# Kernel tuning notes

Hardware: AMD Instinct MI355X
Metric: run time of the kernel (lower is better)

## Reference

```python
import jax, jax.numpy as jnp
import numpy as np

B, H, S, DK = 2, 16, 2048, 128


def setup_inputs() -> dict:
    key = jax.random.key(0)
    kq, kk, kv = jax.random.split(key, 3)
    return {
        "queries": jax.random.normal(kq, (B, H, S, DK), dtype=jnp.float32),
        "keys": jax.random.normal(kk, (B, H, S, DK), dtype=jnp.float32),
        "values": jax.random.normal(kv, (B, H, S, DK), dtype=jnp.float32),
        "d_k": DK,
    }


def reference(queries, keys, values, d_k):
    # scores: [B, H, Sq, Sk] = Q @ K^T / sqrt(d_k)
    scale = 1.0 / np.sqrt(float(d_k)).astype(np.float32)
    scores = jnp.einsum("bhqd,bhkd->bhqk", queries, keys) * scale
    weights = jax.nn.softmax(scores, axis=-1)
    return jnp.einsum("bhqk,bhkd->bhqd", weights, values)
```

## Files before the change

### kernel.cpp

```cpp
#include <hip/hip_runtime.h>
#include <hip/hip_bf16.h>

#define SREF 2048
#define DHEAD 128
#define KVBLK 64
#define NTHREADS 256
#define NTILES (SREF / KVBLK)
#define PSTR 72
#define QSCALE 0.12751743f
#define THRLOG 8.0f

typedef short bf16x8 __attribute__((ext_vector_type(8)));
typedef float f32x4 __attribute__((ext_vector_type(4)));
typedef float f32x16 __attribute__((ext_vector_type(16)));

typedef const __attribute__((address_space(1))) void* gas_t;
typedef __attribute__((address_space(3))) void* las_t;

__device__ __forceinline__ ushort f2bf(float x) {
    unsigned u = __builtin_bit_cast(unsigned, x);
    u += 0x7fffu + ((u >> 16) & 1u);
    return (ushort)(u >> 16);
}

__device__ __forceinline__ float fexp2(float x) {
#if __has_builtin(__builtin_amdgcn_exp2f)
    return __builtin_amdgcn_exp2f(x);
#else
    return exp2f(x);
#endif
}

__device__ __forceinline__ unsigned cvtpk(float lo, float hi) {
    unsigned r;
    asm("v_cvt_pk_bf16_f32 %0, %1, %2" : "=v"(r) : "v"(lo), "v"(hi));
    return r;
}

__global__ __launch_bounds__(NTHREADS) void preconv_kernel(
    const float* __restrict__ K, const float* __restrict__ V,
    ushort* __restrict__ Kb, ushort* __restrict__ VTb)
{
    __shared__ ushort T[DHEAD * PSTR];
    const int t  = threadIdx.x;
    const int bh = blockIdx.y;
    const int s0 = blockIdx.x * KVBLK;
    const size_t base = (size_t)bh * SREF * DHEAD;

    const float* kb = K + base + (size_t)s0 * DHEAD;
    ushort* kout = Kb + base + (size_t)s0 * DHEAD;
    #pragma unroll
    for (int i = 0; i < 8; ++i) {
        int idx = t + i * NTHREADS;
        float4 f = *(const float4*)(kb + idx * 4);
        ushort4 h; h.x = f2bf(f.x); h.y = f2bf(f.y); h.z = f2bf(f.z); h.w = f2bf(f.w);
        *(ushort4*)(kout + idx * 4) = h;
    }

    const float* vb = V + base + (size_t)s0 * DHEAD;
    #pragma unroll
    for (int i = 0; i < 8; ++i) {
        const int key = (t & 31) + 32 * (i & 1);
        const int d4  = (t >> 5) + 8 * (i >> 1);
        float4 f = *(const float4*)(vb + key * DHEAD + d4 * 4);
        T[(d4 * 4 + 0) * PSTR + key] = f2bf(f.x);
        T[(d4 * 4 + 1) * PSTR + key] = f2bf(f.y);
        T[(d4 * 4 + 2) * PSTR + key] = f2bf(f.z);
        T[(d4 * 4 + 3) * PSTR + key] = f2bf(f.w);
    }
    __syncthreads();

    ushort* vt = VTb + (size_t)bh * DHEAD * SREF + s0;
    #pragma unroll
    for (int i = 0; i < 4; ++i) {
        int idx = t + i * NTHREADS;
        int d = idx >> 3;
        int c = (idx & 7) * 8;
        bf16x8 v = *(const bf16x8*)&T[d * PSTR + c];
        *(bf16x8*)(vt + (size_t)d * SREF + c) = v;
    }
}

__global__ __launch_bounds__(NTHREADS, 2) void attn_fwd_kernel(
    const float* __restrict__ Q, const ushort* __restrict__ Kb,
    const ushort* __restrict__ VTb, float* __restrict__ O)
{
    __shared__ __align__(16) char smem[67584];

    const int t    = threadIdx.x;
    const int lane = t & 63;
    const int wv   = t >> 6;
    const int hi   = lane >> 5;
    const int q5   = lane & 31;
    const int swz  = (lane & 7) << 4;

    const int bh = blockIdx.y;
    const int q0 = blockIdx.x * 128;
    const size_t base = (size_t)bh * SREF * DHEAD;

    bf16x8 qf[8];
    {
        const float* qrow = Q + base + (size_t)(q0 + wv * 32 + q5) * DHEAD;
        #pragma unroll
        for (int dk = 0; dk < 8; ++dk) {
            const int d0 = dk * 16 + hi * 8;
            float4 a = *(const float4*)(qrow + d0);
            float4 b = *(const float4*)(qrow + d0 + 4);
            bf16x8 f;
            f[0] = (short)f2bf(a.x * QSCALE); f[1] = (short)f2bf(a.y * QSCALE);
            f[2] = (short)f2bf(a.z * QSCALE); f[3] = (short)f2bf(a.w * QSCALE);
            f[4] = (short)f2bf(b.x * QSCALE); f[5] = (short)f2bf(b.y * QSCALE);
            f[6] = (short)f2bf(b.z * QSCALE); f[7] = (short)f2bf(b.w * QSCALE);
            qf[dk] = f;
        }
    }

    const char* ksrcb = (const char*)(Kb + base);
    const char* vsrcb = (const char*)(VTb + (size_t)bh * DHEAD * SREF);

    const int kbaseL = q5 * 256 + ((hi * 16) ^ swz);
    const int vbaseL = q5 * 128 + ((hi * 16) ^ swz);

#define STAGE(b, kv0) do {                                                      \
    const char* kt_ = ksrcb + (size_t)(kv0) * (DHEAD * 2);                      \
    const char* vt_ = vsrcb + (size_t)(kv0) * 2;                                \
    _Pragma("unroll")                                                           \
    for (int i_ = 0; i_ < 4; ++i_) {                                            \
        int L_ = t * 16 + i_ * 4096;                                            \
        int r_ = L_ >> 8;                                                       \
        __builtin_amdgcn_global_load_lds(                                       \
            (gas_t)(const void*)(kt_ + (L_ ^ ((r_ & 7) << 4))),                 \
            (las_t)(void*)(smem + (b) * 16384 + L_), 16, 0, 0);                 \
    }                                                                           \
    _Pragma("unroll")                                                           \
    for (int i_ = 0; i_ < 4; ++i_) {                                            \
        int L_ = t * 16 + i_ * 4096;                                            \
        int d_ = L_ >> 7;                                                       \
        int c_ = L_ & 127;                                                      \
        __builtin_amdgcn_global_load_lds(                                       \
            (gas_t)(const void*)(vt_ + (size_t)d_ * (SREF * 2) + (c_ ^ ((d_ & 7) << 4))), \
            (las_t)(void*)(smem + 32768 + (b) * 16384 + L_), 16, 0, 0);         \
    }                                                                           \
} while (0)

    float mrun = -1e30f, lsum = 0.0f;
    f32x16 acc[4];
    #pragma unroll
    for (int db = 0; db < 4; ++db)
        #pragma unroll
        for (int i = 0; i < 16; ++i) acc[db][i] = 0.0f;

    STAGE(0, 0);
    int buf = 0;

    for (int tt = 0; tt < NTILES; ++tt) {
        if (tt + 1 < NTILES) {
            STAGE(buf ^ 1, (tt + 1) * KVBLK);
            asm volatile("s_waitcnt vmcnt(8)" ::: "memory");
        } else {
            asm volatile("s_waitcnt vmcnt(0)" ::: "memory");
        }
        __builtin_amdgcn_s_barrier();
        __builtin_amdgcn_sched_barrier(0);

        const int kO = buf * 16384;
        const int vO = 32768 + buf * 16384;

        f32x16 s0, s1;
        #pragma unroll
        for (int i = 0; i < 16; ++i) { s0[i] = 0.0f; s1[i] = 0.0f; }
        __builtin_amdgcn_s_setprio(1);
        #pragma unroll
        for (int dk = 0; dk < 8; ++dk) {
            bf16x8 kf0 = *(const bf16x8*)(smem + kO + (kbaseL ^ (dk << 5)));
            s0 = __builtin_amdgcn_mfma_f32_32x32x16_bf16(kf0, qf[dk], s0, 0, 0, 0);
            bf16x8 kf1 = *(const bf16x8*)(smem + kO + 8192 + (kbaseL ^ (dk << 5)));
            s1 = __builtin_amdgcn_mfma_f32_32x32x16_bf16(kf1, qf[dk], s1, 0, 0, 0);
        }
        __builtin_amdgcn_s_setprio(0);

        float pmax = s0[0];
        #pragma unroll
        for (int i = 1; i < 16; ++i) pmax = fmaxf(pmax, s0[i]);
        #pragma unroll
        for (int i = 0; i < 16; ++i) pmax = fmaxf(pmax, s1[i]);
        pmax = fmaxf(pmax, __shfl_xor(pmax, 32));

        if (!__all(pmax <= mrun + THRLOG)) {
            const float mnew  = fmaxf(mrun, pmax);
            const float alpha = fexp2(mrun - mnew);
            mrun = mnew;
            lsum *= alpha;
            #pragma unroll
            for (int db = 0; db < 4; ++db)
                #pragma unroll
                for (int i = 0; i < 16; ++i) acc[db][i] *= alpha;
        }

        float rs = 0.0f;
        #pragma unroll
        for (int i = 0; i < 16; ++i) { s0[i] = fexp2(s0[i] - mrun); rs += s0[i]; }
        #pragma unroll
        for (int i = 0; i < 16; ++i) { s1[i] = fexp2(s1[i] - mrun); rs += s1[i]; }
        rs += __shfl_xor(rs, 32);
        lsum += rs;

        bf16x8 pa[4];
        #pragma unroll
        for (int kb = 0; kb < 2; ++kb) {
            #pragma unroll
            for (int c = 0; c < 2; ++c) {
                float p0 = (kb ? s1[8*c+0] : s0[8*c+0]);
                float p1 = (kb ? s1[8*c+1] : s0[8*c+1]);
                float p2 = (kb ? s1[8*c+2] : s0[8*c+2]);
                float p3 = (kb ? s1[8*c+3] : s0[8*c+3]);
                float p4 = (kb ? s1[8*c+4] : s0[8*c+4]);
                float p5 = (kb ? s1[8*c+5] : s0[8*c+5]);
                float p6 = (kb ? s1[8*c+6] : s0[8*c+6]);
                float p7 = (kb ? s1[8*c+7] : s0[8*c+7]);
                unsigned x0 = cvtpk(p0, p1);
                unsigned x1 = cvtpk(p2, p3);
                unsigned y0 = cvtpk(p4, p5);
                unsigned y1 = cvtpk(p6, p7);
                asm volatile("v_permlane32_swap_b32 %0, %1" : "+v"(x0), "+v"(y0));
                asm volatile("v_permlane32_swap_b32 %0, %1" : "+v"(x1), "+v"(y1));
                union { unsigned u[4]; bf16x8 v; } U;
                U.u[0] = x0; U.u[1] = x1; U.u[2] = y0; U.u[3] = y1;
                pa[kb * 2 + c] = U.v;
            }
        }

        __builtin_amdgcn_s_setprio(1);
        #pragma unroll
        for (int db = 0; db < 4; ++db) {
            #pragma unroll
            for (int ks = 0; ks < 4; ++ks) {
                bf16x8 vf = *(const bf16x8*)(smem + vO + db * 4096 + (vbaseL ^ (ks << 5)));
                acc[db] = __builtin_amdgcn_mfma_f32_32x32x16_bf16(vf, pa[ks], acc[db], 0, 0, 0);
            }
        }
        __builtin_amdgcn_s_setprio(0);

        __builtin_amdgcn_sched_barrier(0);
        __builtin_amdgcn_s_barrier();
        buf ^= 1;
    }

    __syncthreads();

    const float inv = 1.0f / lsum;
    const int eb = wv * 16896;
    #pragma unroll
    for (int db = 0; db < 4; ++db) {
        #pragma unroll
        for (int c = 0; c < 4; ++c) {
            f32x4 v;
            v[0] = acc[db][4*c+0] * inv;
            v[1] = acc[db][4*c+1] * inv;
            v[2] = acc[db][4*c+2] * inv;
            v[3] = acc[db][4*c+3] * inv;
            *(f32x4*)(smem + eb + q5 * 528 + db * 128 + c * 32 + hi * 16) = v;
        }
    }
    #pragma unroll
    for (int i = 0; i < 16; ++i) {
        const int flat  = lane + i * 64;
        const int row   = flat >> 5;
        const int chunk = flat & 31;
        f32x4 v = *(const f32x4*)(smem + eb + row * 528 + chunk * 16);
        *(f32x4*)(O + base + (size_t)(q0 + wv * 32 + row) * DHEAD + chunk * 4) = v;
    }
#undef STAGE
}

__global__ __launch_bounds__(NTHREADS) void attn_fwd_fallback(
    const float* __restrict__ Q, const float* __restrict__ K,
    const float* __restrict__ V, float* __restrict__ O)
{
    __shared__ ushort Ksh[KVBLK * 136];
    __shared__ ushort Vsh[DHEAD * 72];
    __shared__ ushort Psh[4][16 * PSTR];

    const int t    = threadIdx.x;
    const int lane = t & 63;
    const int wv   = t >> 6;
    const int lq   = lane & 15;
    const int kh   = lane >> 4;

    const int bh = blockIdx.y;
    const int q0 = blockIdx.x * 64;
    const size_t base = (size_t)bh * SREF * DHEAD;

    const float scale = 0.08838834764831845f;
    bf16x8 qf[4];
    {
        const float* qrow = Q + base + (size_t)(q0 + wv * 16 + lq) * DHEAD;
        #pragma unroll
        for (int kk = 0; kk < 4; ++kk) {
            const int d0 = kk * 32 + kh * 8;
            float4 a = *(const float4*)(qrow + d0);
            float4 b = *(const float4*)(qrow + d0 + 4);
            bf16x8 f;
            f[0] = (short)f2bf(a.x * scale); f[1] = (short)f2bf(a.y * scale);
            f[2] = (short)f2bf(a.z * scale); f[3] = (short)f2bf(a.w * scale);
            f[4] = (short)f2bf(b.x * scale); f[5] = (short)f2bf(b.y * scale);
            f[6] = (short)f2bf(b.z * scale); f[7] = (short)f2bf(b.w * scale);
            qf[kk] = f;
        }
    }

    float mrun[4], lrun[4];
    f32x4 acc_o[8];
    #pragma unroll
    for (int r = 0; r < 4; ++r) { mrun[r] = -1e30f; lrun[r] = 0.0f; }
    #pragma unroll
    for (int db = 0; db < 8; ++db) acc_o[db] = (f32x4){0.f, 0.f, 0.f, 0.f};

    for (int kv0 = 0; kv0 < SREF; kv0 += KVBLK) {
        __syncthreads();
        const float* kbase = K + base + (size_t)kv0 * DHEAD;
        #pragma unroll
        for (int i = 0; i < 8; ++i) {
            const int idx = t + i * NTHREADS;
            const int row = idx >> 5;
            const int c4  = idx & 31;
            float4 f = *(const float4*)(kbase + row * DHEAD + c4 * 4);
            ushort4 h;
            h.x = f2bf(f.x); h.y = f2bf(f.y); h.z = f2bf(f.z); h.w = f2bf(f.w);
            *(ushort4*)&Ksh[row * 136 + c4 * 4] = h;
        }
        const float* vbase = V + base + (size_t)kv0 * DHEAD;
        #pragma unroll
        for (int i = 0; i < 8; ++i) {
            const int key = (t & 31) + 32 * (i & 1);
            const int d4  = (t >> 5) + 8 * (i >> 1);
            float4 f = *(const float4*)(vbase + key * DHEAD + d4 * 4);
            Vsh[(d4 * 4 + 0) * 72 + key] = f2bf(f.x);
            Vsh[(d4 * 4 + 1) * 72 + key] = f2bf(f.y);
            Vsh[(d4 * 4 + 2) * 72 + key] = f2bf(f.z);
            Vsh[(d4 * 4 + 3) * 72 + key] = f2bf(f.w);
        }
        __syncthreads();

        f32x4 accs[4];
        #pragma unroll
        for (int nb = 0; nb < 4; ++nb) accs[nb] = (f32x4){0.f, 0.f, 0.f, 0.f};
        #pragma unroll
        for (int kk = 0; kk < 4; ++kk) {
            #pragma unroll
            for (int nb = 0; nb < 4; ++nb) {
                bf16x8 kf = *(const bf16x8*)&Ksh[(nb * 16 + lq) * 136 + kk * 32 + kh * 8];
                accs[nb] = __builtin_amdgcn_mfma_f32_16x16x32_bf16(qf[kk], kf, accs[nb], 0, 0, 0);
            }
        }

        float ps[4][4];
        #pragma unroll
        for (int r = 0; r < 4; ++r) {
            float v = fmaxf(fmaxf(accs[0][r], accs[1][r]), fmaxf(accs[2][r], accs[3][r]));
            #pragma unroll
            for (int mk = 1; mk < 16; mk <<= 1) v = fmaxf(v, __shfl_xor(v, mk));
            const float mnew  = fmaxf(mrun[r], v);
            const float alpha = __expf(mrun[r] - mnew);
            mrun[r] = mnew;
            float rs = 0.0f;
            #pragma unroll
            for (int nb = 0; nb < 4; ++nb) {
                const float p = __expf(accs[nb][r] - mnew);
                ps[nb][r] = p;
                rs += p;
            }
            #pragma unroll
            for (int mk = 1; mk < 16; mk <<= 1) rs += __shfl_xor(rs, mk);
            lrun[r] = lrun[r] * alpha + rs;
            #pragma unroll
            for (int db = 0; db < 8; ++db) acc_o[db][r] *= alpha;
        }

        #pragma unroll
        for (int nb = 0; nb < 4; ++nb)
            #pragma unroll
            for (int r = 0; r < 4; ++r)
                Psh[wv][(kh * 4 + r) * PSTR + nb * 16 + lq] = f2bf(ps[nb][r]);

        #pragma unroll
        for (int ks = 0; ks < 2; ++ks) {
            bf16x8 pa = *(const bf16x8*)&Psh[wv][lq * PSTR + ks * 32 + kh * 8];
            #pragma unroll
            for (int db = 0; db < 8; ++db) {
                bf16x8 vf = *(const bf16x8*)&Vsh[(db * 16 + lq) * 72 + ks * 32 + kh * 8];
                acc_o[db] = __builtin_amdgcn_mfma_f32_16x16x32_bf16(pa, vf, acc_o[db], 0, 0, 0);
            }
        }
    }

    #pragma unroll
    for (int r = 0; r < 4; ++r) {
        const float inv = 1.0f / lrun[r];
        float* orow = O + base + (size_t)(q0 + wv * 16 + kh * 4 + r) * DHEAD;
        #pragma unroll
        for (int db = 0; db < 8; ++db)
            orow[db * 16 + lq] = acc_o[db][r] * inv;
    }
}

extern "C" void kernel_launch(void* const* d_in, const int* in_sizes, int n_in,
                              void* d_out, int out_size, void* d_ws, size_t ws_size,
                              hipStream_t stream) {
    const float* Q = (const float*)d_in[0];
    const float* K = (const float*)d_in[1];
    const float* V = (const float*)d_in[2];
    float* O = (float*)d_out;
    const int BH = in_sizes[0] / (SREF * DHEAD);
    const size_t nel = (size_t)BH * SREF * DHEAD;

    if (ws_size >= 2 * nel * sizeof(ushort)) {
        ushort* Kb  = (ushort*)d_ws;
        ushort* VTb = Kb + nel;
        preconv_kernel<<<dim3(SREF / KVBLK, BH), NTHREADS, 0, stream>>>(K, V, Kb, VTb);
        attn_fwd_kernel<<<dim3(SREF / 128, BH), NTHREADS, 0, stream>>>(Q, Kb, VTb, O);
    } else {
        attn_fwd_fallback<<<dim3(SREF / 64, BH), NTHREADS, 0, stream>>>(Q, K, V, O);
    }
}
```

Before: 100.7 us.

## Software-pipeline attention loop: overlap next QK^T with current softmax and PV

Restructures the main KV loop into a two-tile ping-pong pipeline. The QK^T MFMAs for tile t+1 are issued between the softmax and the PV MFMAs of tile t, and K and V loads are staged separately so K runs one tile ahead. The goal is to hide the softmax VALU and exp latency behind matrix work. It also splits the row-sum reduction into independent accumulators and defers the cross-half lane shuffle of lsum to the epilogue. In exchange it needs more live registers (two score sets) and a full vmcnt(0) wait at each phase, which could cut occupancy or expose load latency.

```diff
diff --git a/kernel.cpp b/kernel.cpp
--- a/kernel.cpp
+++ b/kernel.cpp
@@ -78,6 +78,67 @@
         int c = (idx & 7) * 8;
         bf16x8 v = *(const bf16x8*)&T[d * PSTR + c];
         *(bf16x8*)(vt + (size_t)d * SREF + c) = v;
+    }
+}
+
+__device__ __forceinline__ void softmax_step(
+    f32x16& s0, f32x16& s1, float& mrun, float& lsumh,
+    f32x16* acc, bf16x8* pa)
+{
+    float m0[8];
+    #pragma unroll
+    for (int i = 0; i < 8; ++i)
+        m0[i] = fmaxf(fmaxf(s0[i], s0[i + 8]), fmaxf(s1[i], s1[i + 8]));
+    float pmax = fmaxf(fmaxf(fmaxf(m0[0], m0[1]), fmaxf(m0[2], m0[3])),
+                       fmaxf(fmaxf(m0[4], m0[5]), fmaxf(m0[6], m0[7])));
+    pmax = fmaxf(pmax, __shfl_xor(pmax, 32));
+
+    if (!__all(pmax <= mrun + THRLOG)) {
+        const float mnew  = fmaxf(mrun, pmax);
+        const float alpha = fexp2(mrun - mnew);
+        mrun = mnew;
+        lsumh *= alpha;
+        #pragma unroll
+        for (int db = 0; db < 4; ++db)
+            #pragma unroll
+            for (int i = 0; i < 16; ++i) acc[db][i] *= alpha;
+    }
+
+    float r0 = 0.f, r1 = 0.f, r2 = 0.f, r3 = 0.f;
+    #pragma unroll
+    for (int i = 0; i < 16; i += 4) {
+        s0[i]   = fexp2(s0[i]   - mrun); r0 += s0[i];
+        s0[i+1] = fexp2(s0[i+1] - mrun); r1 += s0[i+1];
+        s0[i+2] = fexp2(s0[i+2] - mrun); r2 += s0[i+2];
+        s0[i+3] = fexp2(s0[i+3] - mrun); r3 += s0[i+3];
+    }
+    #pragma unroll
+    for (int i = 0; i < 16; i += 4) {
+        s1[i]   = fexp2(s1[i]   - mrun); r0 += s1[i];
+        s1[i+1] = fexp2(s1[i+1] - mrun); r1 += s1[i+1];
+        s1[i+2] = fexp2(s1[i+2] - mrun); r2 += s1[i+2];
+        s1[i+3] = fexp2(s1[i+3] - mrun); r3 += s1[i+3];
+    }
+    lsumh += (r0 + r1) + (r2 + r3);
+
+    #pragma unroll
+    for (int kb = 0; kb < 2; ++kb) {
+        #pragma unroll
+        for (int c = 0; c < 2; ++c) {
+            unsigned x0, x1, y0, y1;
+            if (kb == 0) {
+                x0 = cvtpk(s0[8*c+0], s0[8*c+1]); x1 = cvtpk(s0[8*c+2], s0[8*c+3]);
+                y0 = cvtpk(s0[8*c+4], s0[8*c+5]); y1 = cvtpk(s0[8*c+6], s0[8*c+7]);
+            } else {
+                x0 = cvtpk(s1[8*c+0], s1[8*c+1]); x1 = cvtpk(s1[8*c+2], s1[8*c+3]);
+                y0 = cvtpk(s1[8*c+4], s1[8*c+5]); y1 = cvtpk(s1[8*c+6], s1[8*c+7]);
+            }
+            asm volatile("v_permlane32_swap_b32 %0, %1" : "+v"(x0), "+v"(y0));
+            asm volatile("v_permlane32_swap_b32 %0, %1" : "+v"(x1), "+v"(y1));
+            union { unsigned u[4]; bf16x8 v; } U;
+            U.u[0] = x0; U.u[1] = x1; U.u[2] = y0; U.u[3] = y1;
+            pa[kb * 2 + c] = U.v;
+        }
     }
 }
 
@@ -121,17 +182,23 @@
     const int kbaseL = q5 * 256 + ((hi * 16) ^ swz);
     const int vbaseL = q5 * 128 + ((hi * 16) ^ swz);
 
-#define STAGE(b, kv0) do {                                                      \
+#define KOFF(b) ((b) * 16384)
+#define VOFF(b) (32768 + (b) * 16384)
+
+#define STAGE_K(b, kv0) do {                                                    \
     const char* kt_ = ksrcb + (size_t)(kv0) * (DHEAD * 2);                      \
-    const char* vt_ = vsrcb + (size_t)(kv0) * 2;                                \
     _Pragma("unroll")                                                           \
     for (int i_ = 0; i_ < 4; ++i_) {                                            \
         int L_ = t * 16 + i_ * 4096;                                            \
         int r_ = L_ >> 8;                                                       \
         __builtin_amdgcn_global_load_lds(                                       \
             (gas_t)(const void*)(kt_ + (L_ ^ ((r_ & 7) << 4))),                 \
-            (las_t)(void*)(smem + (b) * 16384 + L_), 16, 0, 0);                 \
+            (las_t)(void*)(smem + KOFF(b) + L_), 16, 0, 0);                     \
     }                                                                           \
+} while (0)
+
+#define STAGE_V(b, kv0) do {                                                    \
+    const char* vt_ = vsrcb + (size_t)(kv0) * 2;                                \
     _Pragma("unroll")                                                           \
     for (int i_ = 0; i_ < 4; ++i_) {                                            \
         int L_ = t * 16 + i_ * 4096;                                            \
@@ -139,116 +206,87 @@
         int c_ = L_ & 127;                                                      \
         __builtin_amdgcn_global_load_lds(                                       \
             (gas_t)(const void*)(vt_ + (size_t)d_ * (SREF * 2) + (c_ ^ ((d_ & 7) << 4))), \
-            (las_t)(void*)(smem + 32768 + (b) * 16384 + L_), 16, 0, 0);         \
+            (las_t)(void*)(smem + VOFF(b) + L_), 16, 0, 0);                     \
     }                                                                           \
 } while (0)
 
-    float mrun = -1e30f, lsum = 0.0f;
+#define QK_REGION(sd0, sd1, kO_) do {                                           \
+    _Pragma("unroll")                                                           \
+    for (int i_ = 0; i_ < 16; ++i_) { sd0[i_] = 0.f; sd1[i_] = 0.f; }           \
+    _Pragma("unroll")                                                           \
+    for (int dk_ = 0; dk_ < 8; ++dk_) {                                         \
+        bf16x8 kf0 = *(const bf16x8*)(smem + (kO_) + (kbaseL ^ (dk_ << 5)));    \
+        sd0 = __builtin_amdgcn_mfma_f32_32x32x16_bf16(kf0, qf[dk_], sd0, 0, 0, 0); \
+        bf16x8 kf1 = *(const bf16x8*)(smem + (kO_) + 8192 + (kbaseL ^ (dk_ << 5))); \
+        sd1 = __builtin_amdgcn_mfma_f32_32x32x16_bf16(kf1, qf[dk_], sd1, 0, 0, 0); \
+    }                                                                           \
+} while (0)
+
+#define PV_REGION(pa_, vO_) do {                                                \
+    __builtin_amdgcn_s_setprio(1);                                              \
+    _Pragma("unroll")                                                           \
+    for (int db_ = 0; db_ < 4; ++db_) {                                         \
+        _Pragma("unroll")                                                       \
+        for (int ks_ = 0; ks_ < 4; ++ks_) {                                     \
+            bf16x8 vf = *(const bf16x8*)(smem + (vO_) + db_ * 4096 + (vbaseL ^ (ks_ << 5))); \
+            acc[db_] = __builtin_amdgcn_mfma_f32_32x32x16_bf16(vf, pa_[ks_], acc[db_], 0, 0, 0); \
+        }                                                                       \
+    }                                                                           \
+    __builtin_amdgcn_s_setprio(0);                                              \
+} while (0)
+
+#define PHASE_SYNC() do {                                                       \
+    asm volatile("s_waitcnt vmcnt(0)" ::: "memory");                            \
+    __builtin_amdgcn_s_barrier();                                               \
+    __builtin_amdgcn_sched_barrier(0);                                          \
+} while (0)
+
+    float mrun = -1e30f, lsumh = 0.0f;
     f32x16 acc[4];
     #pragma unroll
     for (int db = 0; db < 4; ++db)
         #pragma unroll
         for (int i = 0; i < 16; ++i) acc[db][i] = 0.0f;
 
-    STAGE(0, 0);
-    int buf = 0;
-
-    for (int tt = 0; tt < NTILES; ++tt) {
-        if (tt + 1 < NTILES) {
-            STAGE(buf ^ 1, (tt + 1) * KVBLK);
-            asm volatile("s_waitcnt vmcnt(8)" ::: "memory");
-        } else {
-            asm volatile("s_waitcnt vmcnt(0)" ::: "memory");
-        }
-        __builtin_amdgcn_s_barrier();
-        __builtin_amdgcn_sched_barrier(0);
-
-        const int kO = buf * 16384;
-        const int vO = 32768 + buf * 16384;
-
-        f32x16 s0, s1;
-        #pragma unroll
-        for (int i = 0; i < 16; ++i) { s0[i] = 0.0f; s1[i] = 0.0f; }
-        __builtin_amdgcn_s_setprio(1);
-        #pragma unroll
-        for (int dk = 0; dk < 8; ++dk) {
-            bf16x8 kf0 = *(const bf16x8*)(smem + kO + (kbaseL ^ (dk << 5)));
-            s0 = __builtin_amdgcn_mfma_f32_32x32x16_bf16(kf0, qf[dk], s0, 0, 0, 0);
-            bf16x8 kf1 = *(const bf16x8*)(smem + kO + 8192 + (kbaseL ^ (dk << 5)));
-            s1 = __builtin_amdgcn_mfma_f32_32x32x16_bf16(kf1, qf[dk], s1, 0, 0, 0);
-        }
-        __builtin_amdgcn_s_setprio(0);
-
-        float pmax = s0[0];
-        #pragma unroll
-        for (int i = 1; i < 16; ++i) pmax = fmaxf(pmax, s0[i]);
-        #pragma unroll
-        for (int i = 0; i < 16; ++i) pmax = fmaxf(pmax, s1[i]);
-        pmax = fmaxf(pmax, __shfl_xor(pmax, 32));
-
-        if (!__all(pmax <= mrun + THRLOG)) {
-            const float mnew  = fmaxf(mrun, pmax);
-            const float alpha = fexp2(mrun - mnew);
-            mrun = mnew;
-            lsum *= alpha;
-            #pragma unroll
-            for (int db = 0; db < 4; ++db)
-                #pragma unroll
-                for (int i = 0; i < 16; ++i) acc[db][i] *= alpha;
-        }
-
-        float rs = 0.0f;
-        #pragma unroll
-        for (int i = 0; i < 16; ++i) { s0[i] = fexp2(s0[i] - mrun); rs += s0[i]; }
-        #pragma unroll
-        for (int i = 0; i < 16; ++i) { s1[i] = fexp2(s1[i] - mrun); rs += s1[i]; }
-        rs += __shfl_xor(rs, 32);
-        lsum += rs;
-
-        bf16x8 pa[4];
-        #pragma unroll
-        for (int kb = 0; kb < 2; ++kb) {
-            #pragma unroll
-            for (int c = 0; c < 2; ++c) {
-                float p0 = (kb ? s1[8*c+0] : s0[8*c+0]);
-                float p1 = (kb ? s1[8*c+1] : s0[8*c+1]);
-                float p2 = (kb ? s1[8*c+2] : s0[8*c+2]);
-                float p3 = (kb ? s1[8*c+3] : s0[8*c+3]);
-                float p4 = (kb ? s1[8*c+4] : s0[8*c+4]);
-                float p5 = (kb ? s1[8*c+5] : s0[8*c+5]);
-                float p6 = (kb ? s1[8*c+6] : s0[8*c+6]);
-                float p7 = (kb ? s1[8*c+7] : s0[8*c+7]);
-                unsigned x0 = cvtpk(p0, p1);
-                unsigned x1 = cvtpk(p2, p3);
-                unsigned y0 = cvtpk(p4, p5);
-                unsigned y1 = cvtpk(p6, p7);
-                asm volatile("v_permlane32_swap_b32 %0, %1" : "+v"(x0), "+v"(y0));
-                asm volatile("v_permlane32_swap_b32 %0, %1" : "+v"(x1), "+v"(y1));
-                union { unsigned u[4]; bf16x8 v; } U;
-                U.u[0] = x0; U.u[1] = x1; U.u[2] = y0; U.u[3] = y1;
-                pa[kb * 2 + c] = U.v;
-            }
-        }
-
-        __builtin_amdgcn_s_setprio(1);
-        #pragma unroll
-        for (int db = 0; db < 4; ++db) {
-            #pragma unroll
-            for (int ks = 0; ks < 4; ++ks) {
-                bf16x8 vf = *(const bf16x8*)(smem + vO + db * 4096 + (vbaseL ^ (ks << 5)));
-                acc[db] = __builtin_amdgcn_mfma_f32_32x32x16_bf16(vf, pa[ks], acc[db], 0, 0, 0);
-            }
-        }
-        __builtin_amdgcn_s_setprio(0);
-
-        __builtin_amdgcn_sched_barrier(0);
-        __builtin_amdgcn_s_barrier();
-        buf ^= 1;
-    }
+    f32x16 sA0, sA1, sB0, sB1;
+    bf16x8 pa[4];
+
+    STAGE_K(0, 0);
+    STAGE_K(1, KVBLK);
+    STAGE_V(0, 0);
+    asm volatile("s_waitcnt vmcnt(16)" ::: "memory");
+    __builtin_amdgcn_s_barrier();
+    __builtin_amdgcn_sched_barrier(0);
+    QK_REGION(sA0, sA1, KOFF(0));
+
+    for (int u = 0; u < 15; ++u) {
+        const int t0 = 2 * u;
+        PHASE_SYNC();
+        STAGE_K(0, (t0 + 2) * KVBLK);
+        STAGE_V(1, (t0 + 1) * KVBLK);
+        softmax_step(sA0, sA1, mrun, lsumh, acc, pa);
+        QK_REGION(sB0, sB1, KOFF(1));
+        PV_REGION(pa, VOFF(0));
+        PHASE_SYNC();
+        STAGE_K(1, (t0 + 3) * KVBLK);
+        STAGE_V(0, (t0 + 2) * KVBLK);
+        softmax_step(sB0, sB1, mrun, lsumh, acc, pa);
+        QK_REGION(sA0, sA1, KOFF(0));
+        PV_REGION(pa, VOFF(1));
+    }
+    PHASE_SYNC();
+    STAGE_V(1, 31 * KVBLK);
+    softmax_step(sA0, sA1, mrun, lsumh, acc, pa);
+    QK_REGION(sB0, sB1, KOFF(1));
+    PV_REGION(pa, VOFF(0));
+    PHASE_SYNC();
+    softmax_step(sB0, sB1, mrun, lsumh, acc, pa);
+    PV_REGION(pa, VOFF(1));
 
     __syncthreads();
 
-    const float inv = 1.0f / lsum;
+    const float lsum = lsumh + __shfl_xor(lsumh, 32);
+    const float inv  = 1.0f / lsum;
     const int eb = wv * 16896;
     #pragma unroll
     for (int db = 0; db < 4; ++db) {
@@ -270,7 +308,13 @@
         f32x4 v = *(const f32x4*)(smem + eb + row * 528 + chunk * 16);
         *(f32x4*)(O + base + (size_t)(q0 + wv * 32 + row) * DHEAD + chunk * 4) = v;
     }
-#undef STAGE
+#undef STAGE_K
+#undef STAGE_V
+#undef QK_REGION
+#undef PV_REGION
+#undef PHASE_SYNC
+#undef KOFF
+#undef VOFF
 }
 
 __global__ __launch_bounds__(NTHREADS) void attn_fwd_fallback(
```

Measured after the change: 104.4 us. +3.6%, slower.

## Halve KV tile to 32 keys, retile V layout, raise occupancy to four blocks

Applied to the files above, without the earlier changes.

Shrinks the key/value tile per iteration from 64 to 32 keys. This halves shared memory per block and raises the launch bound to four blocks per CU. The preconvert kernel now writes V transposed into contiguous 32-key tiles so each stage is one linear 8 KB chunk, and the row sum is kept per half-wave and combined at the end. The epilogue staging is serialized across two rounds to fit the smaller shared buffer. In exchange there are twice as many barriers and loop iterations, and register pressure under the tighter bound may cause spills.

```diff
diff --git a/kernel.cpp b/kernel.cpp
--- a/kernel.cpp
+++ b/kernel.cpp
@@ -3,7 +3,7 @@
 
 #define SREF 2048
 #define DHEAD 128
-#define KVBLK 64
+#define KVBLK 32
 #define NTHREADS 256
 #define NTILES (SREF / KVBLK)
 #define PSTR 72
@@ -39,12 +39,12 @@
 
 __global__ __launch_bounds__(NTHREADS) void preconv_kernel(
     const float* __restrict__ K, const float* __restrict__ V,
-    ushort* __restrict__ Kb, ushort* __restrict__ VTb)
+    ushort* __restrict__ Kb, ushort* __restrict__ VTt)
 {
     __shared__ ushort T[DHEAD * PSTR];
     const int t  = threadIdx.x;
     const int bh = blockIdx.y;
-    const int s0 = blockIdx.x * KVBLK;
+    const int s0 = blockIdx.x * 64;
     const size_t base = (size_t)bh * SREF * DHEAD;
 
     const float* kb = K + base + (size_t)s0 * DHEAD;
@@ -70,29 +70,32 @@
     }
     __syncthreads();
 
-    ushort* vt = VTb + (size_t)bh * DHEAD * SREF + s0;
+    ushort* vt = VTt + ((size_t)bh * (SREF / 32) + (size_t)(s0 >> 5)) * 4096;
     #pragma unroll
     for (int i = 0; i < 4; ++i) {
-        int idx = t + i * NTHREADS;
-        int d = idx >> 3;
-        int c = (idx & 7) * 8;
-        bf16x8 v = *(const bf16x8*)&T[d * PSTR + c];
-        *(bf16x8*)(vt + (size_t)d * SREF + c) = v;
-    }
-}
-
-__global__ __launch_bounds__(NTHREADS, 2) void attn_fwd_kernel(
+        int idx  = t + i * NTHREADS;
+        int ht   = idx >> 9;
+        int w    = idx & 511;
+        int r    = w >> 3;
+        int half = (w >> 2) & 1;
+        int kc   = (w & 3) * 8;
+        bf16x8 v = *(const bf16x8*)&T[(r + 64 * half) * PSTR + 32 * ht + kc];
+        *(bf16x8*)(vt + (size_t)ht * 4096 + r * 64 + half * 32 + kc) = v;
+    }
+}
+
+__global__ __launch_bounds__(NTHREADS, 4) void attn_fwd_kernel(
     const float* __restrict__ Q, const ushort* __restrict__ Kb,
-    const ushort* __restrict__ VTb, float* __restrict__ O)
+    const ushort* __restrict__ VTt, float* __restrict__ O)
 {
-    __shared__ __align__(16) char smem[67584];
+    __shared__ __align__(16) char smem[33792];
 
     const int t    = threadIdx.x;
     const int lane = t & 63;
     const int wv   = t >> 6;
     const int hi   = lane >> 5;
     const int q5   = lane & 31;
-    const int swz  = (lane & 7) << 4;
+    const int sw   = (q5 & 7) << 4;
 
     const int bh = blockIdx.y;
     const int q0 = blockIdx.x * 128;
@@ -116,34 +119,36 @@
     }
 
     const char* ksrcb = (const char*)(Kb + base);
-    const char* vsrcb = (const char*)(VTb + (size_t)bh * DHEAD * SREF);
-
-    const int kbaseL = q5 * 256 + ((hi * 16) ^ swz);
-    const int vbaseL = q5 * 128 + ((hi * 16) ^ swz);
-
-#define STAGE(b, kv0) do {                                                      \
-    const char* kt_ = ksrcb + (size_t)(kv0) * (DHEAD * 2);                      \
-    const char* vt_ = vsrcb + (size_t)(kv0) * 2;                                \
+    const char* vsrcb = (const char*)(VTt + (size_t)bh * (SREF / 32) * 4096);
+
+    const int kbase2 = q5 * 256 + ((hi * 16) ^ sw);
+    const int vbase2 = q5 * 128 + ((hi * 16) ^ sw);
+
+#define KOFF(b) ((b) * 8192)
+#define VOFF(b) (16384 + (b) * 8192)
+
+#define STAGE(b, tt) do {                                                       \
+    const char* kt_ = ksrcb + (size_t)(tt) * 8192;                              \
+    const char* vt_ = vsrcb + (size_t)(tt) * 8192;                              \
     _Pragma("unroll")                                                           \
-    for (int i_ = 0; i_ < 4; ++i_) {                                            \
+    for (int i_ = 0; i_ < 2; ++i_) {                                            \
         int L_ = t * 16 + i_ * 4096;                                            \
         int r_ = L_ >> 8;                                                       \
         __builtin_amdgcn_global_load_lds(                                       \
             (gas_t)(const void*)(kt_ + (L_ ^ ((r_ & 7) << 4))),                 \
-            (las_t)(void*)(smem + (b) * 16384 + L_), 16, 0, 0);                 \
+            (las_t)(void*)(smem + KOFF(b) + L_), 16, 0, 0);                     \
     }                                                                           \
     _Pragma("unroll")                                                           \
-    for (int i_ = 0; i_ < 4; ++i_) {                                            \
+    for (int i_ = 0; i_ < 2; ++i_) {                                            \
         int L_ = t * 16 + i_ * 4096;                                            \
-        int d_ = L_ >> 7;                                                       \
-        int c_ = L_ & 127;                                                      \
+        int r_ = L_ >> 7;                                                       \
         __builtin_amdgcn_global_load_lds(                                       \
-            (gas_t)(const void*)(vt_ + (size_t)d_ * (SREF * 2) + (c_ ^ ((d_ & 7) << 4))), \
-            (las_t)(void*)(smem + 32768 + (b) * 16384 + L_), 16, 0, 0);         \
+            (gas_t)(const void*)(vt_ + (L_ ^ ((r_ & 7) << 4))),                 \
+            (las_t)(void*)(smem + VOFF(b) + L_), 16, 0, 0);                     \
     }                                                                           \
 } while (0)
 
-    float mrun = -1e30f, lsum = 0.0f;
+    float mrun = -1e30f, lsumh = 0.0f;
     f32x16 acc[4];
     #pragma unroll
     for (int db = 0; db < 4; ++db)
@@ -155,87 +160,77 @@
 
     for (int tt = 0; tt < NTILES; ++tt) {
         if (tt + 1 < NTILES) {
-            STAGE(buf ^ 1, (tt + 1) * KVBLK);
-            asm volatile("s_waitcnt vmcnt(8)" ::: "memory");
+            STAGE(buf ^ 1, tt + 1);
+            asm volatile("s_waitcnt vmcnt(4)" ::: "memory");
         } else {
             asm volatile("s_waitcnt vmcnt(0)" ::: "memory");
         }
         __builtin_amdgcn_s_barrier();
         __builtin_amdgcn_sched_barrier(0);
 
-        const int kO = buf * 16384;
-        const int vO = 32768 + buf * 16384;
-
-        f32x16 s0, s1;
-        #pragma unroll
-        for (int i = 0; i < 16; ++i) { s0[i] = 0.0f; s1[i] = 0.0f; }
+        const int kO = KOFF(buf);
+        const int vO = VOFF(buf);
+
+        f32x16 s0;
+        #pragma unroll
+        for (int i = 0; i < 16; ++i) s0[i] = 0.0f;
         __builtin_amdgcn_s_setprio(1);
         #pragma unroll
         for (int dk = 0; dk < 8; ++dk) {
-            bf16x8 kf0 = *(const bf16x8*)(smem + kO + (kbaseL ^ (dk << 5)));
-            s0 = __builtin_amdgcn_mfma_f32_32x32x16_bf16(kf0, qf[dk], s0, 0, 0, 0);
-            bf16x8 kf1 = *(const bf16x8*)(smem + kO + 8192 + (kbaseL ^ (dk << 5)));
-            s1 = __builtin_amdgcn_mfma_f32_32x32x16_bf16(kf1, qf[dk], s1, 0, 0, 0);
+            bf16x8 kf = *(const bf16x8*)(smem + kO + (kbase2 ^ (dk << 5)));
+            s0 = __builtin_amdgcn_mfma_f32_32x32x16_bf16(kf, qf[dk], s0, 0, 0, 0);
         }
         __builtin_amdgcn_s_setprio(0);
 
-        float pmax = s0[0];
-        #pragma unroll
-        for (int i = 1; i < 16; ++i) pmax = fmaxf(pmax, s0[i]);
-        #pragma unroll
-        for (int i = 0; i < 16; ++i) pmax = fmaxf(pmax, s1[i]);
+        float m0[8];
+        #pragma unroll
+        for (int i = 0; i < 8; ++i) m0[i] = fmaxf(s0[i], s0[i + 8]);
+        float pmax = fmaxf(fmaxf(fmaxf(m0[0], m0[1]), fmaxf(m0[2], m0[3])),
+                           fmaxf(fmaxf(m0[4], m0[5]), fmaxf(m0[6], m0[7])));
         pmax = fmaxf(pmax, __shfl_xor(pmax, 32));
 
         if (!__all(pmax <= mrun + THRLOG)) {
             const float mnew  = fmaxf(mrun, pmax);
             const float alpha = fexp2(mrun - mnew);
             mrun = mnew;
-            lsum *= alpha;
+            lsumh *= alpha;
             #pragma unroll
             for (int db = 0; db < 4; ++db)
                 #pragma unroll
                 for (int i = 0; i < 16; ++i) acc[db][i] *= alpha;
         }
 
-        float rs = 0.0f;
-        #pragma unroll
-        for (int i = 0; i < 16; ++i) { s0[i] = fexp2(s0[i] - mrun); rs += s0[i]; }
-        #pragma unroll
-        for (int i = 0; i < 16; ++i) { s1[i] = fexp2(s1[i] - mrun); rs += s1[i]; }
-        rs += __shfl_xor(rs, 32);
-        lsum += rs;
-
-        bf16x8 pa[4];
-        #pragma unroll
-        for (int kb = 0; kb < 2; ++kb) {
-            #pragma unroll
-            for (int c = 0; c < 2; ++c) {
-                float p0 = (kb ? s1[8*c+0] : s0[8*c+0]);
-                float p1 = (kb ? s1[8*c+1] : s0[8*c+1]);
-                float p2 = (kb ? s1[8*c+2] : s0[8*c+2]);
-                float p3 = (kb ? s1[8*c+3] : s0[8*c+3]);
-                float p4 = (kb ? s1[8*c+4] : s0[8*c+4]);
-                float p5 = (kb ? s1[8*c+5] : s0[8*c+5]);
-                float p6 = (kb ? s1[8*c+6] : s0[8*c+6]);
-                float p7 = (kb ? s1[8*c+7] : s0[8*c+7]);
-                unsigned x0 = cvtpk(p0, p1);
-                unsigned x1 = cvtpk(p2, p3);
-                unsigned y0 = cvtpk(p4, p5);
-                unsigned y1 = cvtpk(p6, p7);
-                asm volatile("v_permlane32_swap_b32 %0, %1" : "+v"(x0), "+v"(y0));
-                asm volatile("v_permlane32_swap_b32 %0, %1" : "+v"(x1), "+v"(y1));
-                union { unsigned u[4]; bf16x8 v; } U;
-                U.u[0] = x0; U.u[1] = x1; U.u[2] = y0; U.u[3] = y1;
-                pa[kb * 2 + c] = U.v;
-            }
+        float r0 = 0.f, r1 = 0.f, r2 = 0.f, r3 = 0.f;
+        #pragma unroll
+        for (int i = 0; i < 16; i += 4) {
+            s0[i]   = fexp2(s0[i]   - mrun); r0 += s0[i];
+            s0[i+1] = fexp2(s0[i+1] - mrun); r1 += s0[i+1];
+            s0[i+2] = fexp2(s0[i+2] - mrun); r2 += s0[i+2];
+            s0[i+3] = fexp2(s0[i+3] - mrun); r3 += s0[i+3];
+        }
+        lsumh += (r0 + r1) + (r2 + r3);
+
+        bf16x8 pa[2];
+        #pragma unroll
+        for (int c = 0; c < 2; ++c) {
+            unsigned x0 = cvtpk(s0[8*c+0], s0[8*c+1]);
+            unsigned x1 = cvtpk(s0[8*c+2], s0[8*c+3]);
+            unsigned y0 = cvtpk(s0[8*c+4], s0[8*c+5]);
+            unsigned y1 = cvtpk(s0[8*c+6], s0[8*c+7]);
+            asm volatile("v_permlane32_swap_b32 %0, %1" : "+v"(x0), "+v"(y0));
+            asm volatile("v_permlane32_swap_b32 %0, %1" : "+v"(x1), "+v"(y1));
+            union { unsigned u[4]; bf16x8 v; } U;
+            U.u[0] = x0; U.u[1] = x1; U.u[2] = y0; U.u[3] = y1;
+            pa[c] = U.v;
         }
 
         __builtin_amdgcn_s_setprio(1);
         #pragma unroll
         for (int db = 0; db < 4; ++db) {
-            #pragma unroll
-            for (int ks = 0; ks < 4; ++ks) {
-                bf16x8 vf = *(const bf16x8*)(smem + vO + db * 4096 + (vbaseL ^ (ks << 5)));
+            const int vb = vbase2 + (db & 1) * 4096;
+            #pragma unroll
+            for (int ks = 0; ks < 2; ++ks) {
+                bf16x8 vf = *(const bf16x8*)(smem + vO + (vb ^ ((db >> 1) << 6) ^ (ks << 5)));
                 acc[db] = __builtin_amdgcn_mfma_f32_32x32x16_bf16(vf, pa[ks], acc[db], 0, 0, 0);
             }
         }
@@ -247,37 +242,46 @@
     }
 
     __syncthreads();
-
-    const float inv = 1.0f / lsum;
-    const int eb = wv * 16896;
-    #pragma unroll
-    for (int db = 0; db < 4; ++db) {
-        #pragma unroll
-        for (int c = 0; c < 4; ++c) {
-            f32x4 v;
-            v[0] = acc[db][4*c+0] * inv;
-            v[1] = acc[db][4*c+1] * inv;
-            v[2] = acc[db][4*c+2] * inv;
-            v[3] = acc[db][4*c+3] * inv;
-            *(f32x4*)(smem + eb + q5 * 528 + db * 128 + c * 32 + hi * 16) = v;
-        }
-    }
-    #pragma unroll
-    for (int i = 0; i < 16; ++i) {
-        const int flat  = lane + i * 64;
-        const int row   = flat >> 5;
-        const int chunk = flat & 31;
-        f32x4 v = *(const f32x4*)(smem + eb + row * 528 + chunk * 16);
-        *(f32x4*)(O + base + (size_t)(q0 + wv * 32 + row) * DHEAD + chunk * 4) = v;
+    const float lsum = lsumh + __shfl_xor(lsumh, 32);
+    const float inv  = 1.0f / lsum;
+
+    #pragma unroll
+    for (int round = 0; round < 2; ++round) {
+        if ((wv >> 1) == round) {
+            const int eb = (wv & 1) * 16896;
+            #pragma unroll
+            for (int db = 0; db < 4; ++db) {
+                #pragma unroll
+                for (int c = 0; c < 4; ++c) {
+                    f32x4 v;
+                    v[0] = acc[db][4*c+0] * inv;
+                    v[1] = acc[db][4*c+1] * inv;
+                    v[2] = acc[db][4*c+2] * inv;
+                    v[3] = acc[db][4*c+3] * inv;
+                    *(f32x4*)(smem + eb + q5 * 528 + db * 128 + c * 32 + hi * 16) = v;
+                }
+            }
+            #pragma unroll
+            for (int i = 0; i < 16; ++i) {
+                const int flat  = lane + i * 64;
+                const int row   = flat >> 5;
+                const int chunk = flat & 31;
+                f32x4 v = *(const f32x4*)(smem + eb + row * 528 + chunk * 16);
+                *(f32x4*)(O + base + (size_t)(q0 + wv * 32 + row) * DHEAD + chunk * 4) = v;
+            }
+        }
+        __syncthreads();
     }
 #undef STAGE
+#undef KOFF
+#undef VOFF
 }
 
 __global__ __launch_bounds__(NTHREADS) void attn_fwd_fallback(
     const float* __restrict__ Q, const float* __restrict__ K,
     const float* __restrict__ V, float* __restrict__ O)
 {
-    __shared__ ushort Ksh[KVBLK * 136];
+    __shared__ ushort Ksh[64 * 136];
     __shared__ ushort Vsh[DHEAD * 72];
     __shared__ ushort Psh[4][16 * PSTR];
 
@@ -316,7 +320,7 @@
     #pragma unroll
     for (int db = 0; db < 8; ++db) acc_o[db] = (f32x4){0.f, 0.f, 0.f, 0.f};
 
-    for (int kv0 = 0; kv0 < SREF; kv0 += KVBLK) {
+    for (int kv0 = 0; kv0 < SREF; kv0 += 64) {
         __syncthreads();
         const float* kbase = K + base + (size_t)kv0 * DHEAD;
         #pragma unroll
@@ -416,9 +420,9 @@
 
     if (ws_size >= 2 * nel * sizeof(ushort)) {
         ushort* Kb  = (ushort*)d_ws;
-        ushort* VTb = Kb + nel;
-        preconv_kernel<<<dim3(SREF / KVBLK, BH), NTHREADS, 0, stream>>>(K, V, Kb, VTb);
-        attn_fwd_kernel<<<dim3(SREF / 128, BH), NTHREADS, 0, stream>>>(Q, Kb, VTb, O);
+        ushort* VTt = Kb + nel;
+        preconv_kernel<<<dim3(SREF / 64, BH), NTHREADS, 0, stream>>>(K, V, Kb, VTt);
+        attn_fwd_kernel<<<dim3(SREF / 128, BH), NTHREADS, 0, stream>>>(Q, Kb, VTt, O);
     } else {
         attn_fwd_fallback<<<dim3(SREF / 64, BH), NTHREADS, 0, stream>>>(Q, K, V, O);
     }
```

Result: slower. 174.7 us (+73.4%).

## Use 128-key tiles with single-buffered K/V staging split across phases

Applied to the files above, without the earlier changes.

Doubles the KV tile to 128 keys and replaces the double-buffered combined K+V stage with single K and V buffers. The next K tile is loaded during the softmax and PV phase, and the next V tile is loaded after PV, so each tile gets half as many barriers and loop iterations. The row max and sum reductions become tree-shaped with split accumulators. The epilogue now writes output in two rounds to fit the smaller LDS. The risks are higher register pressure from four score tiles plus eight P fragments, and less slack to hide load latency with a single buffer.

```diff
diff --git a/kernel.cpp b/kernel.cpp
--- a/kernel.cpp
+++ b/kernel.cpp
@@ -3,7 +3,7 @@
 
 #define SREF 2048
 #define DHEAD 128
-#define KVBLK 64
+#define KVBLK 128
 #define NTHREADS 256
 #define NTILES (SREF / KVBLK)
 #define PSTR 72
@@ -44,7 +44,7 @@
     __shared__ ushort T[DHEAD * PSTR];
     const int t  = threadIdx.x;
     const int bh = blockIdx.y;
-    const int s0 = blockIdx.x * KVBLK;
+    const int s0 = blockIdx.x * 64;
     const size_t base = (size_t)bh * SREF * DHEAD;
 
     const float* kb = K + base + (size_t)s0 * DHEAD;
@@ -85,14 +85,14 @@
     const float* __restrict__ Q, const ushort* __restrict__ Kb,
     const ushort* __restrict__ VTb, float* __restrict__ O)
 {
-    __shared__ __align__(16) char smem[67584];
+    __shared__ __align__(16) char smem[65536];
 
     const int t    = threadIdx.x;
     const int lane = t & 63;
     const int wv   = t >> 6;
     const int hi   = lane >> 5;
     const int q5   = lane & 31;
-    const int swz  = (lane & 7) << 4;
+    const int sw   = (q5 & 7) << 4;
 
     const int bh = blockIdx.y;
     const int q0 = blockIdx.x * 128;
@@ -118,110 +118,121 @@
     const char* ksrcb = (const char*)(Kb + base);
     const char* vsrcb = (const char*)(VTb + (size_t)bh * DHEAD * SREF);
 
-    const int kbaseL = q5 * 256 + ((hi * 16) ^ swz);
-    const int vbaseL = q5 * 128 + ((hi * 16) ^ swz);
-
-#define STAGE(b, kv0) do {                                                      \
-    const char* kt_ = ksrcb + (size_t)(kv0) * (DHEAD * 2);                      \
-    const char* vt_ = vsrcb + (size_t)(kv0) * 2;                                \
+    const int kbaseL = q5 * 256 + ((hi * 16) ^ sw);
+
+#define STAGE_K(tt) do {                                                        \
+    const char* kt_ = ksrcb + (size_t)(tt) * 32768;                             \
     _Pragma("unroll")                                                           \
-    for (int i_ = 0; i_ < 4; ++i_) {                                            \
+    for (int i_ = 0; i_ < 8; ++i_) {                                            \
         int L_ = t * 16 + i_ * 4096;                                            \
         int r_ = L_ >> 8;                                                       \
         __builtin_amdgcn_global_load_lds(                                       \
             (gas_t)(const void*)(kt_ + (L_ ^ ((r_ & 7) << 4))),                 \
-            (las_t)(void*)(smem + (b) * 16384 + L_), 16, 0, 0);                 \
+            (las_t)(void*)(smem + L_), 16, 0, 0);                               \
     }                                                                           \
+} while (0)
+
+#define STAGE_V(tt) do {                                                        \
+    const char* vt_ = vsrcb + (size_t)(tt) * 256;                               \
     _Pragma("unroll")                                                           \
-    for (int i_ = 0; i_ < 4; ++i_) {                                            \
+    for (int i_ = 0; i_ < 8; ++i_) {                                            \
         int L_ = t * 16 + i_ * 4096;                                            \
-        int d_ = L_ >> 7;                                                       \
-        int c_ = L_ & 127;                                                      \
+        int d_ = L_ >> 8;                                                       \
+        int c_ = L_ & 255;                                                      \
         __builtin_amdgcn_global_load_lds(                                       \
             (gas_t)(const void*)(vt_ + (size_t)d_ * (SREF * 2) + (c_ ^ ((d_ & 7) << 4))), \
-            (las_t)(void*)(smem + 32768 + (b) * 16384 + L_), 16, 0, 0);         \
+            (las_t)(void*)(smem + 32768 + L_), 16, 0, 0);                       \
     }                                                                           \
 } while (0)
 
-    float mrun = -1e30f, lsum = 0.0f;
+    float mrun = -1e30f, lsumh = 0.0f;
     f32x16 acc[4];
     #pragma unroll
     for (int db = 0; db < 4; ++db)
         #pragma unroll
         for (int i = 0; i < 16; ++i) acc[db][i] = 0.0f;
 
-    STAGE(0, 0);
-    int buf = 0;
+    STAGE_K(0);
+    STAGE_V(0);
 
     for (int tt = 0; tt < NTILES; ++tt) {
-        if (tt + 1 < NTILES) {
-            STAGE(buf ^ 1, (tt + 1) * KVBLK);
-            asm volatile("s_waitcnt vmcnt(8)" ::: "memory");
-        } else {
-            asm volatile("s_waitcnt vmcnt(0)" ::: "memory");
-        }
+        asm volatile("s_waitcnt vmcnt(8)" ::: "memory");
         __builtin_amdgcn_s_barrier();
         __builtin_amdgcn_sched_barrier(0);
 
-        const int kO = buf * 16384;
-        const int vO = 32768 + buf * 16384;
-
-        f32x16 s0, s1;
-        #pragma unroll
-        for (int i = 0; i < 16; ++i) { s0[i] = 0.0f; s1[i] = 0.0f; }
+        f32x16 s0, s1, s2, s3;
+        #pragma unroll
+        for (int i = 0; i < 16; ++i) { s0[i] = 0.f; s1[i] = 0.f; s2[i] = 0.f; s3[i] = 0.f; }
         __builtin_amdgcn_s_setprio(1);
         #pragma unroll
         for (int dk = 0; dk < 8; ++dk) {
-            bf16x8 kf0 = *(const bf16x8*)(smem + kO + (kbaseL ^ (dk << 5)));
+            const int off = kbaseL ^ (dk << 5);
+            bf16x8 kf0 = *(const bf16x8*)(smem + off);
             s0 = __builtin_amdgcn_mfma_f32_32x32x16_bf16(kf0, qf[dk], s0, 0, 0, 0);
-            bf16x8 kf1 = *(const bf16x8*)(smem + kO + 8192 + (kbaseL ^ (dk << 5)));
+            bf16x8 kf1 = *(const bf16x8*)(smem + 8192 + off);
             s1 = __builtin_amdgcn_mfma_f32_32x32x16_bf16(kf1, qf[dk], s1, 0, 0, 0);
+            bf16x8 kf2 = *(const bf16x8*)(smem + 16384 + off);
+            s2 = __builtin_amdgcn_mfma_f32_32x32x16_bf16(kf2, qf[dk], s2, 0, 0, 0);
+            bf16x8 kf3 = *(const bf16x8*)(smem + 24576 + off);
+            s3 = __builtin_amdgcn_mfma_f32_32x32x16_bf16(kf3, qf[dk], s3, 0, 0, 0);
         }
         __builtin_amdgcn_s_setprio(0);
 
-        float pmax = s0[0];
-        #pragma unroll
-        for (int i = 1; i < 16; ++i) pmax = fmaxf(pmax, s0[i]);
-        #pragma unroll
-        for (int i = 0; i < 16; ++i) pmax = fmaxf(pmax, s1[i]);
+        asm volatile("s_waitcnt vmcnt(0)" ::: "memory");
+        __builtin_amdgcn_s_barrier();
+        __builtin_amdgcn_sched_barrier(0);
+        if (tt + 1 < NTILES) STAGE_K(tt + 1);
+
+        float m0[16];
+        #pragma unroll
+        for (int i = 0; i < 16; ++i)
+            m0[i] = fmaxf(fmaxf(s0[i], s1[i]), fmaxf(s2[i], s3[i]));
+        float m1[8];
+        #pragma unroll
+        for (int i = 0; i < 8; ++i) m1[i] = fmaxf(m0[i], m0[i + 8]);
+        float pmax = fmaxf(fmaxf(fmaxf(m1[0], m1[1]), fmaxf(m1[2], m1[3])),
+                           fmaxf(fmaxf(m1[4], m1[5]), fmaxf(m1[6], m1[7])));
         pmax = fmaxf(pmax, __shfl_xor(pmax, 32));
 
         if (!__all(pmax <= mrun + THRLOG)) {
             const float mnew  = fmaxf(mrun, pmax);
             const float alpha = fexp2(mrun - mnew);
             mrun = mnew;
-            lsum *= alpha;
+            lsumh *= alpha;
             #pragma unroll
             for (int db = 0; db < 4; ++db)
                 #pragma unroll
                 for (int i = 0; i < 16; ++i) acc[db][i] *= alpha;
         }
 
-        float rs = 0.0f;
-        #pragma unroll
-        for (int i = 0; i < 16; ++i) { s0[i] = fexp2(s0[i] - mrun); rs += s0[i]; }
-        #pragma unroll
-        for (int i = 0; i < 16; ++i) { s1[i] = fexp2(s1[i] - mrun); rs += s1[i]; }
-        rs += __shfl_xor(rs, 32);
-        lsum += rs;
-
-        bf16x8 pa[4];
+        bf16x8 pa[8];
+        float r0 = 0.f, r1 = 0.f, r2 = 0.f, r3 = 0.f;
+        #pragma unroll
+        for (int i = 0; i < 16; i += 4) {
+            s0[i]   = fexp2(s0[i]   - mrun); r0 += s0[i];
+            s0[i+1] = fexp2(s0[i+1] - mrun); r1 += s0[i+1];
+            s0[i+2] = fexp2(s0[i+2] - mrun); r2 += s0[i+2];
+            s0[i+3] = fexp2(s0[i+3] - mrun); r3 += s0[i+3];
+        }
+        #pragma unroll
+        for (int i = 0; i < 16; i += 4) {
+            s1[i]   = fexp2(s1[i]   - mrun); r0 += s1[i];
+            s1[i+1] = fexp2(s1[i+1] - mrun); r1 += s1[i+1];
+            s1[i+2] = fexp2(s1[i+2] - mrun); r2 += s1[i+2];
+            s1[i+3] = fexp2(s1[i+3] - mrun); r3 += s1[i+3];
+        }
         #pragma unroll
         for (int kb = 0; kb < 2; ++kb) {
             #pragma unroll
             for (int c = 0; c < 2; ++c) {
-                float p0 = (kb ? s1[8*c+0] : s0[8*c+0]);
-                float p1 = (kb ? s1[8*c+1] : s0[8*c+1]);
-                float p2 = (kb ? s1[8*c+2] : s0[8*c+2]);
-                float p3 = (kb ? s1[8*c+3] : s0[8*c+3]);
-                float p4 = (kb ? s1[8*c+4] : s0[8*c+4]);
-                float p5 = (kb ? s1[8*c+5] : s0[8*c+5]);
-                float p6 = (kb ? s1[8*c+6] : s0[8*c+6]);
-                float p7 = (kb ? s1[8*c+7] : s0[8*c+7]);
-                unsigned x0 = cvtpk(p0, p1);
-                unsigned x1 = cvtpk(p2, p3);
-                unsigned y0 = cvtpk(p4, p5);
-                unsigned y1 = cvtpk(p6, p7);
+                unsigned x0, x1, y0, y1;
+                if (kb == 0) {
+                    x0 = cvtpk(s0[8*c+0], s0[8*c+1]); x1 = cvtpk(s0[8*c+2], s0[8*c+3]);
+                    y0 = cvtpk(s0[8*c+4], s0[8*c+5]); y1 = cvtpk(s0[8*c+6], s0[8*c+7]);
+                } else {
+                    x0 = cvtpk(s1[8*c+0], s1[8*c+1]); x1 = cvtpk(s1[8*c+2], s1[8*c+3]);
+                    y0 = cvtpk(s1[8*c+4], s1[8*c+5]); y1 = cvtpk(s1[8*c+6], s1[8*c+7]);
+                }
                 asm volatile("v_permlane32_swap_b32 %0, %1" : "+v"(x0), "+v"(y0));
                 asm volatile("v_permlane32_swap_b32 %0, %1" : "+v"(x1), "+v"(y1));
                 union { unsigned u[4]; bf16x8 v; } U;
@@ -229,55 +240,100 @@
                 pa[kb * 2 + c] = U.v;
             }
         }
+        #pragma unroll
+        for (int i = 0; i < 16; i += 4) {
+            s2[i]   = fexp2(s2[i]   - mrun); r0 += s2[i];
+            s2[i+1] = fexp2(s2[i+1] - mrun); r1 += s2[i+1];
+            s2[i+2] = fexp2(s2[i+2] - mrun); r2 += s2[i+2];
+            s2[i+3] = fexp2(s2[i+3] - mrun); r3 += s2[i+3];
+        }
+        #pragma unroll
+        for (int i = 0; i < 16; i += 4) {
+            s3[i]   = fexp2(s3[i]   - mrun); r0 += s3[i];
+            s3[i+1] = fexp2(s3[i+1] - mrun); r1 += s3[i+1];
+            s3[i+2] = fexp2(s3[i+2] - mrun); r2 += s3[i+2];
+            s3[i+3] = fexp2(s3[i+3] - mrun); r3 += s3[i+3];
+        }
+        #pragma unroll
+        for (int kb = 0; kb < 2; ++kb) {
+            #pragma unroll
+            for (int c = 0; c < 2; ++c) {
+                unsigned x0, x1, y0, y1;
+                if (kb == 0) {
+                    x0 = cvtpk(s2[8*c+0], s2[8*c+1]); x1 = cvtpk(s2[8*c+2], s2[8*c+3]);
+                    y0 = cvtpk(s2[8*c+4], s2[8*c+5]); y1 = cvtpk(s2[8*c+6], s2[8*c+7]);
+                } else {
+                    x0 = cvtpk(s3[8*c+0], s3[8*c+1]); x1 = cvtpk(s3[8*c+2], s3[8*c+3]);
+                    y0 = cvtpk(s3[8*c+4], s3[8*c+5]); y1 = cvtpk(s3[8*c+6], s3[8*c+7]);
+                }
+                asm volatile("v_permlane32_swap_b32 %0, %1" : "+v"(x0), "+v"(y0));
+                asm volatile("v_permlane32_swap_b32 %0, %1" : "+v"(x1), "+v"(y1));
+                union { unsigned u[4]; bf16x8 v; } U;
+                U.u[0] = x0; U.u[1] = x1; U.u[2] = y0; U.u[3] = y1;
+                pa[4 + kb * 2 + c] = U.v;
+            }
+        }
+        lsumh += (r0 + r1) + (r2 + r3);
 
         __builtin_amdgcn_s_setprio(1);
         #pragma unroll
         for (int db = 0; db < 4; ++db) {
-            #pragma unroll
-            for (int ks = 0; ks < 4; ++ks) {
-                bf16x8 vf = *(const bf16x8*)(smem + vO + db * 4096 + (vbaseL ^ (ks << 5)));
+            const int vrow = (db * 32 + q5) * 256 + ((hi * 16) ^ sw);
+            #pragma unroll
+            for (int ks = 0; ks < 8; ++ks) {
+                bf16x8 vf = *(const bf16x8*)(smem + 32768 + (vrow ^ (ks << 5)));
                 acc[db] = __builtin_amdgcn_mfma_f32_32x32x16_bf16(vf, pa[ks], acc[db], 0, 0, 0);
             }
         }
         __builtin_amdgcn_s_setprio(0);
-
         __builtin_amdgcn_sched_barrier(0);
-        __builtin_amdgcn_s_barrier();
-        buf ^= 1;
+
+        if (tt + 1 < NTILES) {
+            __builtin_amdgcn_s_barrier();
+            STAGE_V(tt + 1);
+        }
     }
 
     __syncthreads();
-
-    const float inv = 1.0f / lsum;
-    const int eb = wv * 16896;
-    #pragma unroll
-    for (int db = 0; db < 4; ++db) {
-        #pragma unroll
-        for (int c = 0; c < 4; ++c) {
-            f32x4 v;
-            v[0] = acc[db][4*c+0] * inv;
-            v[1] = acc[db][4*c+1] * inv;
-            v[2] = acc[db][4*c+2] * inv;
-            v[3] = acc[db][4*c+3] * inv;
-            *(f32x4*)(smem + eb + q5 * 528 + db * 128 + c * 32 + hi * 16) = v;
-        }
-    }
-    #pragma unroll
-    for (int i = 0; i < 16; ++i) {
-        const int flat  = lane + i * 64;
-        const int row   = flat >> 5;
-        const int chunk = flat & 31;
-        f32x4 v = *(const f32x4*)(smem + eb + row * 528 + chunk * 16);
-        *(f32x4*)(O + base + (size_t)(q0 + wv * 32 + row) * DHEAD + chunk * 4) = v;
-    }
-#undef STAGE
+    const float lsum = lsumh + __shfl_xor(lsumh, 32);
+    const float inv  = 1.0f / lsum;
+
+    #pragma unroll
+    for (int round = 0; round < 2; ++round) {
+        if ((wv >> 1) == round) {
+            const int eb = (wv & 1) * 16896;
+            #pragma unroll
+            for (int db = 0; db < 4; ++db) {
+                #pragma unroll
+                for (int c = 0; c < 4; ++c) {
+                    f32x4 v;
+                    v[0] = acc[db][4*c+0] * inv;
+                    v[1] = acc[db][4*c+1] * inv;
+                    v[2] = acc[db][4*c+2] * inv;
+                    v[3] = acc[db][4*c+3] * inv;
+                    *(f32x4*)(smem + eb + q5 * 528 + db * 128 + c * 32 + hi * 16) = v;
+                }
+            }
+            #pragma unroll
+            for (int i = 0; i < 16; ++i) {
+                const int flat  = lane + i * 64;
+                const int row   = flat >> 5;
+                const int chunk = flat & 31;
+                f32x4 v = *(const f32x4*)(smem + eb + row * 528 + chunk * 16);
+                *(f32x4*)(O + base + (size_t)(q0 + wv * 32 + row) * DHEAD + chunk * 4) = v;
+            }
+        }
+        __syncthreads();
+    }
+#undef STAGE_K
+#undef STAGE_V
 }
 
 __global__ __launch_bounds__(NTHREADS) void attn_fwd_fallback(
     const float* __restrict__ Q, const float* __restrict__ K,
     const float* __restrict__ V, float* __restrict__ O)
 {
-    __shared__ ushort Ksh[KVBLK * 136];
+    __shared__ ushort Ksh[64 * 136];
     __shared__ ushort Vsh[DHEAD * 72];
     __shared__ ushort Psh[4][16 * PSTR];
 
@@ -316,7 +372,7 @@
     #pragma unroll
     for (int db = 0; db < 8; ++db) acc_o[db] = (f32x4){0.f, 0.f, 0.f, 0.f};
 
-    for (int kv0 = 0; kv0 < SREF; kv0 += KVBLK) {
+    for (int kv0 = 0; kv0 < SREF; kv0 += 64) {
         __syncthreads();
         const float* kbase = K + base + (size_t)kv0 * DHEAD;
         #pragma unroll
@@ -417,7 +473,7 @@
     if (ws_size >= 2 * nel * sizeof(ushort)) {
         ushort* Kb  = (ushort*)d_ws;
         ushort* VTb = Kb + nel;
-        preconv_kernel<<<dim3(SREF / KVBLK, BH), NTHREADS, 0, stream>>>(K, V, Kb, VTb);
+        preconv_kernel<<<dim3(SREF / 64, BH), NTHREADS, 0, stream>>>(K, V, Kb, VTb);
         attn_fwd_kernel<<<dim3(SREF / 128, BH), NTHREADS, 0, stream>>>(Q, Kb, VTb, O);
     } else {
         attn_fwd_fallback<<<dim3(SREF / 64, BH), NTHREADS, 0, stream>>>(Q, K, V, O);
```

After: 99.76 us. Within noise of the previous version (-1.0%).
